# Performance work log

Hardware: AMD Instinct MI355X
Metric: run time of the kernel (lower is better)

## Reference

```python
import jax, jax.numpy as jnp
import numpy as np

N_NODES = 50000
N_EDGES = 800000


def setup_inputs() -> dict:
    key = jax.random.key(0)
    ks = jax.random.split(key, 8)
    x = jax.random.normal(ks[0], (N_NODES, 128), dtype=jnp.float32)
    edge_src = jax.random.randint(ks[1], (N_EDGES,), 0, N_NODES, dtype=jnp.int32)
    edge_dst = jax.random.randint(ks[2], (N_EDGES,), 0, N_NODES, dtype=jnp.int32)
    # normalized-adjacency-style positive edge weights
    edge_weight = jax.random.uniform(ks[3], (N_EDGES,), dtype=jnp.float32)
    # Kipf-style uniform(-stdv, stdv) init, stdv = 1/sqrt(fan_out)
    def w(k, fi, fo):
        stdv = 1.0 / np.sqrt(fo)
        return jax.random.uniform(k, (fi, fo), minval=-stdv, maxval=stdv, dtype=jnp.float32)
    W1 = w(ks[4], 128, 128)
    W2 = w(ks[5], 128, 128)
    W3 = w(ks[6], 128, 64)
    b1 = jnp.zeros((128,), jnp.float32)
    b2 = jnp.zeros((128,), jnp.float32)
    b3 = jnp.zeros((64,), jnp.float32)
    return {"x": x, "edge_src": edge_src, "edge_dst": edge_dst,
            "edge_weight": edge_weight, "W1": W1, "b1": b1,
            "W2": W2, "b2": b2, "W3": W3, "b3": b3}


def reference(x, edge_src, edge_dst, edge_weight, W1, b1, W2, b2, W3, b3):
    N = x.shape[0]

    def graph_conv(h, W, b):
        # support = h @ W  (dense GEMM)
        support = h @ W
        # spmm(adj, support): gather source rows, scale by edge weight,
        # scatter-add into destination rows
        msg = edge_weight[:, None] * support[edge_src]          # [E, d_out]
        agg = jax.ops.segment_sum(msg, edge_dst, num_segments=N)
        return agg + b

    h = jax.nn.relu(graph_conv(x, W1, b1))
    h = jax.nn.relu(graph_conv(h, W2, b2))
    h = graph_conv(h, W3, b3)
    return jax.nn.log_softmax(h, axis=1)
```

## Files before the change

### kernel.cpp

```cpp
#include <hip/hip_runtime.h>
#include <cstdint>
#include <cstddef>

typedef __attribute__((ext_vector_type(8))) short short8v;
typedef __attribute__((ext_vector_type(4))) float f32x4;

__device__ inline uint bf16_rne(float f) {
    uint u = __float_as_uint(f);
    return (u + 0x7fffu + ((u >> 16) & 1u)) >> 16;
}
__device__ inline float bf16lo_to_f(uint v) { return __uint_as_float(v << 16); }
__device__ inline float bf16hi_to_f(uint v) { return __uint_as_float(v & 0xffff0000u); }

#define MAXDEG 64
#define RSV 384
#define EPB 2048

__device__ inline void pack_one(const float* __restrict__ W, ushort* __restrict__ Wp,
                                int NC, int i) {
    int j = i & 7, l = (i >> 3) & 63, kb = (i >> 9) & 3, c = i >> 11;
    int row = kb * 32 + ((l >> 4) & 3) * 8 + j;
    int col = c * 16 + (l & 15);
    Wp[i] = (ushort)bf16_rne(W[row * NC + col]);
}

__global__ __launch_bounds__(256) void part_init_kernel(
        const int* __restrict__ esrc, const int* __restrict__ edst,
        const float* __restrict__ ew, float invN8,
        int* __restrict__ lens, int2* __restrict__ part, int E, int NFB,
        int* __restrict__ cnt, int N,
        const float* __restrict__ W1, ushort* __restrict__ Wp1,
        const float* __restrict__ W2, ushort* __restrict__ Wp2,
        const float* __restrict__ W3, ushort* __restrict__ Wp3) {
    const int b = blockIdx.x;
    if (b >= NFB) {
        const int ZB = (N + 255) >> 8;
        int r = b - NFB;
        if (r < ZB) {
            int i = r * 256 + threadIdx.x;
            if (i < N) cnt[i] = 0;
        } else {
            int p = (r - ZB) * 256 + threadIdx.x;
            if (p < 16384) pack_one(W1, Wp1, 128, p);
            else if (p < 32768) pack_one(W2, Wp2, 128, p - 16384);
            else if (p < 40960) pack_one(W3, Wp3, 64, p - 32768);
        }
        return;
    }
    const int fb = b;
    __shared__ int lcnt[8];
    if (threadIdx.x < 8) lcnt[threadIdx.x] = 0;
    __syncthreads();

    const int lane = threadIdx.x & 63;
    const unsigned long long ltmask = (1ULL << lane) - 1ULL;
    const int base = fb * EPB;

#pragma unroll
    for (int j = 0; j < 8; ++j) {
        int idx = base + j * 256 + threadIdx.x;
        bool valid = idx < E;
        int dv = 0, bk = -1;
        int2 rec;
        if (valid) {
            dv = edst[idx];
            bk = min(7, (int)((float)dv * invN8));
            rec.x = (dv << 16) | esrc[idx];
            rec.y = __float_as_int(ew[idx]);
        }
        int myrank = 0, lanecnt = 0;
#pragma unroll
        for (int k = 0; k < 8; ++k) {
            unsigned long long mk = __ballot(bk == k);
            if (bk == k) myrank = (int)__popcll(mk & ltmask);
            if (lane == k) lanecnt = (int)__popcll(mk);
        }
        int wbase = 0;
        if (lane < 8) wbase = atomicAdd(&lcnt[lane], lanecnt);
        int segbase = __shfl(wbase, (bk < 0) ? 0 : bk);
        if (valid) {
            int pos = segbase + myrank;
            if (pos < RSV) part[((size_t)bk * NFB + fb) * RSV + pos] = rec;
        }
    }
    __syncthreads();
    if (threadIdx.x < 8) lens[fb * 8 + threadIdx.x] = min(lcnt[threadIdx.x], RSV);
}

template <int NC, bool F32IN>
__device__ __forceinline__ void gemm_body(const void* __restrict__ Xin,
                                          const ushort* __restrict__ Wp,
                                          ushort* __restrict__ Out, int M, int bid,
                                          ushort* WL) {
    const int t = threadIdx.x;
    {
        const uint4* srcp = (const uint4*)Wp;
        uint4* dstp = (uint4*)WL;
#pragma unroll
        for (int i = 0; i < NC / 16; ++i) dstp[t + i * 256] = srcp[t + i * 256];
    }
    __syncthreads();

    const int wave = t >> 6, l = t & 63;
    const int lr = l & 15, lh = l >> 4;
    const int rowbase = bid * 64 + wave * 16;
    const int arow_idx = min(rowbase + lr, M - 1);

    short8v a[4];
    if (F32IN) {
        const float* arow = (const float*)Xin + (size_t)arow_idx * 128 + lh * 8;
#pragma unroll
        for (int kb = 0; kb < 4; ++kb) {
            float4 u = *(const float4*)(arow + kb * 32);
            float4 v = *(const float4*)(arow + kb * 32 + 4);
            short8v av;
            av[0] = (short)bf16_rne(u.x); av[1] = (short)bf16_rne(u.y);
            av[2] = (short)bf16_rne(u.z); av[3] = (short)bf16_rne(u.w);
            av[4] = (short)bf16_rne(v.x); av[5] = (short)bf16_rne(v.y);
            av[6] = (short)bf16_rne(v.z); av[7] = (short)bf16_rne(v.w);
            a[kb] = av;
        }
    } else {
        const ushort* arow = (const ushort*)Xin + (size_t)arow_idx * 128 + lh * 8;
#pragma unroll
        for (int kb = 0; kb < 4; ++kb) a[kb] = *(const short8v*)(arow + kb * 32);
    }

    f32x4 acc[NC / 16];
#pragma unroll
    for (int c = 0; c < NC / 16; ++c) acc[c] = (f32x4){0.f, 0.f, 0.f, 0.f};

#pragma unroll
    for (int c = 0; c < NC / 16; ++c)
#pragma unroll
        for (int kb = 0; kb < 4; ++kb) {
            short8v b = *(const short8v*)(WL + ((c * 4 + kb) * 64 + l) * 8);
            acc[c] = __builtin_amdgcn_mfma_f32_16x16x32_bf16(a[kb], b, acc[c], 0, 0, 0);
        }

#pragma unroll
    for (int c = 0; c < NC / 16; ++c)
#pragma unroll
        for (int i = 0; i < 4; ++i) {
            int row = rowbase + lh * 4 + i;
            if (row < M) Out[(size_t)row * NC + c * 16 + lr] = (ushort)bf16_rne(acc[c][i]);
        }
}

template <int NC, bool F32IN>
__global__ __launch_bounds__(256) void gemm_mfma(const void* __restrict__ Xin,
                                                 const ushort* __restrict__ Wp,
                                                 ushort* __restrict__ Out, int M) {
    __shared__ ushort WL[128 * NC];
    gemm_body<NC, F32IN>(Xin, Wp, Out, M, blockIdx.x, WL);
}

__global__ __launch_bounds__(256) void gemm1_scatter_kernel(
        const float* __restrict__ X, const ushort* __restrict__ Wp1,
        ushort* __restrict__ Out, int M, int GG, int NSG,
        const int* __restrict__ lens, const int2* __restrict__ part,
        int* __restrict__ cnt, uint* __restrict__ slots, int NFB) {
    __shared__ ushort WL[128 * 128];
    const int g = blockIdx.x >> 3;
    const int i = blockIdx.x & 7;
    if (((g & 1) == 0) && ((g >> 1) < GG)) {
        gemm_body<128, true>(X, Wp1, Out, M, (g >> 1) * 8 + i, WL);
        return;
    }
    const int gemms_before = min((g + 1) >> 1, GG);
    const int sg = g - gemms_before;
    const int bucket = i;
    for (int seg = sg; seg < NFB; seg += NSG) {
        const int len = lens[seg * 8 + bucket];
        const int2* p = part + ((size_t)bucket * NFB + seg) * RSV;
        for (int r = threadIdx.x; r < len; r += 256) {
            int2 rec = p[r];
            uint dv = (uint)rec.x >> 16;
            uint src = (uint)rec.x & 0xffffu;
            int pos = atomicAdd(&cnt[dv], 1);
            if (pos < MAXDEG)
                slots[(size_t)dv * MAXDEG + pos] =
                    (bf16_rne(__int_as_float(rec.y)) << 16) | src;
        }
    }
}

__global__ void spmm128_kernel(const uint* __restrict__ S, const int* __restrict__ cnt,
                               const uint* __restrict__ slots, const float* __restrict__ bias,
                               uint* __restrict__ Out, int N) {
    const int bucket = blockIdx.x & 7;
    const int bidx = blockIdx.x >> 3;
    const int lo = (int)((long)bucket * N / 8);
    const int hi = (int)((long)(bucket + 1) * N / 8);
    const int node = lo + bidx * 4 + (threadIdx.x >> 6);
    const int lane = threadIdx.x & 63;
    if (node >= hi) return;
    const int e1 = min(cnt[node], MAXDEG);
    const uint* sl = slots + (size_t)node * MAXDEG;
    float ax = 0.f, ay = 0.f;
    int e = 0;

#define EDGE128(pk)                                                  \
    {                                                                \
        uint _p = (pk);                                              \
        float _w = __uint_as_float(_p & 0xffff0000u);                \
        uint _v = S[(size_t)(_p & 0xffffu) * 64 + lane];             \
        ax = fmaf(_w, bf16lo_to_f(_v), ax);                          \
        ay = fmaf(_w, bf16hi_to_f(_v), ay);                          \
    }

    for (; e + 8 <= e1; e += 8) {
        uint4 c0 = *(const uint4*)(sl + e);
        uint4 c1 = *(const uint4*)(sl + e + 4);
        EDGE128(c0.x); EDGE128(c0.y); EDGE128(c0.z); EDGE128(c0.w);
        EDGE128(c1.x); EDGE128(c1.y); EDGE128(c1.z); EDGE128(c1.w);
    }
    for (; e + 4 <= e1; e += 4) {
        uint4 c0 = *(const uint4*)(sl + e);
        EDGE128(c0.x); EDGE128(c0.y); EDGE128(c0.z); EDGE128(c0.w);
    }
    for (; e < e1; ++e) EDGE128(sl[e]);
#undef EDGE128

    float2 bv = ((const float2*)bias)[lane];
    ax = fmaxf(ax + bv.x, 0.f);
    ay = fmaxf(ay + bv.y, 0.f);
    Out[(size_t)node * 64 + lane] = (bf16_rne(ay) << 16) | bf16_rne(ax);
}

__global__ void spmm64_kernel(const uint* __restrict__ S32, const int* __restrict__ cnt,
                              const uint* __restrict__ slots, const float* __restrict__ bias,
                              float* __restrict__ Out, int N) {
    const int bucket = blockIdx.x & 7;
    const int bidx = blockIdx.x >> 3;
    const int lo = (int)((long)bucket * N / 8);
    const int hi = (int)((long)(bucket + 1) * N / 8);
    const int node = lo + bidx * 8 + (threadIdx.x >> 5);
    const int l = threadIdx.x & 31;
    if (node >= hi) return;
    const int e1 = min(cnt[node], MAXDEG);
    const uint* sl = slots + (size_t)node * MAXDEG;
    float a0 = 0.f, a1 = 0.f;
    int e = 0;

#define EDGE64(pk)                                                  \
    {                                                               \
        uint _p = (pk);                                             \
        float _w = __uint_as_float(_p & 0xffff0000u);               \
        uint _v = S32[(size_t)(_p & 0xffffu) * 32 + l];             \
        a0 = fmaf(_w, bf16lo_to_f(_v), a0);                         \
        a1 = fmaf(_w, bf16hi_to_f(_v), a1);                         \
    }

    for (; e + 8 <= e1; e += 8) {
        uint4 c0 = *(const uint4*)(sl + e);
        uint4 c1 = *(const uint4*)(sl + e + 4);
        EDGE64(c0.x); EDGE64(c0.y); EDGE64(c0.z); EDGE64(c0.w);
        EDGE64(c1.x); EDGE64(c1.y); EDGE64(c1.z); EDGE64(c1.w);
    }
    for (; e + 4 <= e1; e += 4) {
        uint4 c0 = *(const uint4*)(sl + e);
        EDGE64(c0.x); EDGE64(c0.y); EDGE64(c0.z); EDGE64(c0.w);
    }
    for (; e < e1; ++e) EDGE64(sl[e]);
#undef EDGE64

    float2 bv = ((const float2*)bias)[l];
    float v0 = a0 + bv.x;
    float v1 = a1 + bv.y;
    float m = fmaxf(v0, v1);
#pragma unroll
    for (int d = 16; d >= 1; d >>= 1) m = fmaxf(m, __shfl_xor(m, d));
    float s = __expf(v0 - m) + __expf(v1 - m);
#pragma unroll
    for (int d = 16; d >= 1; d >>= 1) s += __shfl_xor(s, d);
    float ls = __logf(s);
    float2 o;
    o.x = (v0 - m) - ls;
    o.y = (v1 - m) - ls;
    ((float2*)Out)[(size_t)node * 32 + l] = o;
}


extern "C" void kernel_launch(void* const* d_in, const int* in_sizes, int n_in,
                              void* d_out, int out_size, void* d_ws, size_t ws_size,
                              hipStream_t stream) {
    const float* x  = (const float*)d_in[0];
    const int* esrc = (const int*)d_in[1];
    const int* edst = (const int*)d_in[2];
    const float* ew = (const float*)d_in[3];
    const float* W1 = (const float*)d_in[4];
    const float* b1 = (const float*)d_in[5];
    const float* W2 = (const float*)d_in[6];
    const float* b2 = (const float*)d_in[7];
    const float* W3 = (const float*)d_in[8];
    const float* b3 = (const float*)d_in[9];

    const int N = in_sizes[0] / 128;
    const int E = in_sizes[1];

    char* ws = (char*)d_ws;
    auto alloc = [&](size_t bytes) {
        char* p = ws;
        ws += (bytes + 255) & ~(size_t)255;
        return p;
    };
    const int NFB = (E + EPB - 1) / EPB;
    int* cnt     = (int*)alloc((size_t)N * 4);
    int* lens    = (int*)alloc((size_t)(NFB + 8) * 8 * 4);
    uint* slots  = (uint*)alloc((size_t)N * MAXDEG * 4);
    ushort* Sb   = (ushort*)alloc((size_t)N * 128 * 2);
    ushort* Hb   = (ushort*)alloc((size_t)N * 128 * 2);
    ushort* Wp1  = (ushort*)alloc(128 * 128 * 2);
    ushort* Wp2  = (ushort*)alloc(128 * 128 * 2);
    ushort* Wp3  = (ushort*)alloc(128 * 64 * 2);
    (void)ws_size;
    int2* part = (int2*)Hb;

    const float invN8 = 8.0f / (float)N;
    const int ZB = (N + 255) / 256;
    const int PK = (40960 + 255) / 256;

    part_init_kernel<<<NFB + ZB + PK, 256, 0, stream>>>(
        esrc, edst, ew, invN8, lens, part, E, NFB,
        cnt, N, W1, Wp1, W2, Wp2, W3, Wp3);

    const int GB = (N + 63) / 64;
    const int GG = (GB + 7) / 8;
    const int NSG = 128;
    const int TG = GG + NSG;
    gemm1_scatter_kernel<<<TG * 8, 256, 0, stream>>>(
        x, Wp1, Sb, N, GG, NSG, lens, part, cnt, slots, NFB);

    const int bpb128 = (((N + 7) / 8) + 3) / 4;
    spmm128_kernel<<<bpb128 * 8, 256, 0, stream>>>((const uint*)Sb, cnt, slots, b1, (uint*)Hb, N);

    gemm_mfma<128, false><<<GB, 256, 0, stream>>>(Hb, Wp2, Sb, N);
    spmm128_kernel<<<bpb128 * 8, 256, 0, stream>>>((const uint*)Sb, cnt, slots, b2, (uint*)Hb, N);

    gemm_mfma<64, false><<<GB, 256, 0, stream>>>(Hb, Wp3, Sb, N);
    const int bpb64 = (((N + 7) / 8) + 7) / 8;
    spmm64_kernel<<<bpb64 * 8, 256, 0, stream>>>((const uint*)Sb, cnt, slots, b3, (float*)d_out, N);
}
```

Before: 157.1 us.

## Fuse SpMM aggregation with the following layer's MFMA GEMM per 64-node tile

Replaces the separate spmm128 and gemm_mfma launches with one kernel. Each block aggregates 64 nodes into LDS as bf16 with bias and ReLU, then multiplies that tile by the next layer's packed weights using MFMA and writes the support matrix directly. This drops the round trip of the hidden activation through global memory and two kernel launches. In exchange each block reloads the full weight matrix into LDS, uses more LDS per block, and runs at 512 threads, which may lower occupancy for the latency-bound gather.

Result: slower. 161.2 us (+2.6%).

```diff
diff --git a/kernel.cpp b/kernel.cpp
--- a/kernel.cpp
+++ b/kernel.cpp
@@ -147,14 +147,6 @@
         }
 }
 
-template <int NC, bool F32IN>
-__global__ __launch_bounds__(256) void gemm_mfma(const void* __restrict__ Xin,
-                                                 const ushort* __restrict__ Wp,
-                                                 ushort* __restrict__ Out, int M) {
-    __shared__ ushort WL[128 * NC];
-    gemm_body<NC, F32IN>(Xin, Wp, Out, M, blockIdx.x, WL);
-}
-
 __global__ __launch_bounds__(256) void gemm1_scatter_kernel(
         const float* __restrict__ X, const ushort* __restrict__ Wp1,
         ushort* __restrict__ Out, int M, int GG, int NSG,
@@ -185,47 +177,89 @@
     }
 }
 
-__global__ void spmm128_kernel(const uint* __restrict__ S, const int* __restrict__ cnt,
-                               const uint* __restrict__ slots, const float* __restrict__ bias,
-                               uint* __restrict__ Out, int N) {
+template <int NC>
+__global__ __launch_bounds__(512) void spmm_gemm_kernel(
+        const uint* __restrict__ S, const int* __restrict__ cnt,
+        const uint* __restrict__ slots, const float* __restrict__ bias,
+        const ushort* __restrict__ Wp, ushort* __restrict__ Out, int N) {
+    __shared__ uint HL[64][68];
+    __shared__ ushort WL[128 * NC];
+    const int t = threadIdx.x;
+    {
+        const uint4* srcp = (const uint4*)Wp;
+        uint4* dstp = (uint4*)WL;
+#pragma unroll
+        for (int i = 0; i < NC / 32; ++i) dstp[t + i * 512] = srcp[t + i * 512];
+    }
     const int bucket = blockIdx.x & 7;
-    const int bidx = blockIdx.x >> 3;
+    const int tile = blockIdx.x >> 3;
     const int lo = (int)((long)bucket * N / 8);
     const int hi = (int)((long)(bucket + 1) * N / 8);
-    const int node = lo + bidx * 4 + (threadIdx.x >> 6);
-    const int lane = threadIdx.x & 63;
-    if (node >= hi) return;
-    const int e1 = min(cnt[node], MAXDEG);
-    const uint* sl = slots + (size_t)node * MAXDEG;
-    float ax = 0.f, ay = 0.f;
-    int e = 0;
-
+    const int base = lo + tile * 64;
+    const int wave = t >> 6, lane = t & 63;
+
+    float2 bv = ((const float2*)bias)[lane];
+#pragma unroll
+    for (int r8 = 0; r8 < 8; ++r8) {
+        const int r = wave * 8 + r8;
+        const int node = base + r;
+        float ax = 0.f, ay = 0.f;
+        if (node < hi) {
+            const int e1 = min(cnt[node], MAXDEG);
+            const uint* sl = slots + (size_t)node * MAXDEG;
+            int e = 0;
 #define EDGE128(pk)                                                  \
-    {                                                                \
-        uint _p = (pk);                                              \
-        float _w = __uint_as_float(_p & 0xffff0000u);                \
-        uint _v = S[(size_t)(_p & 0xffffu) * 64 + lane];             \
-        ax = fmaf(_w, bf16lo_to_f(_v), ax);                          \
-        ay = fmaf(_w, bf16hi_to_f(_v), ay);                          \
-    }
-
-    for (; e + 8 <= e1; e += 8) {
-        uint4 c0 = *(const uint4*)(sl + e);
-        uint4 c1 = *(const uint4*)(sl + e + 4);
-        EDGE128(c0.x); EDGE128(c0.y); EDGE128(c0.z); EDGE128(c0.w);
-        EDGE128(c1.x); EDGE128(c1.y); EDGE128(c1.z); EDGE128(c1.w);
-    }
-    for (; e + 4 <= e1; e += 4) {
-        uint4 c0 = *(const uint4*)(sl + e);
-        EDGE128(c0.x); EDGE128(c0.y); EDGE128(c0.z); EDGE128(c0.w);
-    }
-    for (; e < e1; ++e) EDGE128(sl[e]);
+            {                                                        \
+                uint _p = (pk);                                      \
+                float _w = __uint_as_float(_p & 0xffff0000u);        \
+                uint _v = S[(size_t)(_p & 0xffffu) * 64 + lane];     \
+                ax = fmaf(_w, bf16lo_to_f(_v), ax);                  \
+                ay = fmaf(_w, bf16hi_to_f(_v), ay);                  \
+            }
+            for (; e + 8 <= e1; e += 8) {
+                uint4 c0 = *(const uint4*)(sl + e);
+                uint4 c1 = *(const uint4*)(sl + e + 4);
+                EDGE128(c0.x); EDGE128(c0.y); EDGE128(c0.z); EDGE128(c0.w);
+                EDGE128(c1.x); EDGE128(c1.y); EDGE128(c1.z); EDGE128(c1.w);
+            }
+            for (; e + 4 <= e1; e += 4) {
+                uint4 c0 = *(const uint4*)(sl + e);
+                EDGE128(c0.x); EDGE128(c0.y); EDGE128(c0.z); EDGE128(c0.w);
+            }
+            for (; e < e1; ++e) EDGE128(sl[e]);
 #undef EDGE128
-
-    float2 bv = ((const float2*)bias)[lane];
-    ax = fmaxf(ax + bv.x, 0.f);
-    ay = fmaxf(ay + bv.y, 0.f);
-    Out[(size_t)node * 64 + lane] = (bf16_rne(ay) << 16) | bf16_rne(ax);
+            ax = fmaxf(ax + bv.x, 0.f);
+            ay = fmaxf(ay + bv.y, 0.f);
+        }
+        HL[r][lane] = (bf16_rne(ay) << 16) | bf16_rne(ax);
+    }
+    __syncthreads();
+
+    const int lr = lane & 15, lh = lane >> 4;
+    const int rt = wave & 3;
+    const int nct = NC / 16;
+    const int ct0 = (wave >> 2) * (nct / 2);
+
+    short8v a[4];
+#pragma unroll
+    for (int kb = 0; kb < 4; ++kb)
+        a[kb] = *(const short8v*)&HL[rt * 16 + lr][kb * 16 + lh * 4];
+
+#pragma unroll
+    for (int c = 0; c < NC / 32; ++c) {
+        const int ct = ct0 + c;
+        f32x4 acc = (f32x4){0.f, 0.f, 0.f, 0.f};
+#pragma unroll
+        for (int kb = 0; kb < 4; ++kb) {
+            short8v b = *(const short8v*)(WL + ((ct * 4 + kb) * 64 + lane) * 8);
+            acc = __builtin_amdgcn_mfma_f32_16x16x32_bf16(a[kb], b, acc, 0, 0, 0);
+        }
+#pragma unroll
+        for (int i = 0; i < 4; ++i) {
+            int row = base + rt * 16 + lh * 4 + i;
+            if (row < hi) Out[(size_t)row * NC + ct * 16 + lr] = (ushort)bf16_rne(acc[i]);
+        }
+    }
 }
 
 __global__ void spmm64_kernel(const uint* __restrict__ S32, const int* __restrict__ cnt,
@@ -332,13 +366,14 @@
     gemm1_scatter_kernel<<<TG * 8, 256, 0, stream>>>(
         x, Wp1, Sb, N, GG, NSG, lens, part, cnt, slots, NFB);
 
-    const int bpb128 = (((N + 7) / 8) + 3) / 4;
-    spmm128_kernel<<<bpb128 * 8, 256, 0, stream>>>((const uint*)Sb, cnt, slots, b1, (uint*)Hb, N);
-
-    gemm_mfma<128, false><<<GB, 256, 0, stream>>>(Hb, Wp2, Sb, N);
-    spmm128_kernel<<<bpb128 * 8, 256, 0, stream>>>((const uint*)Sb, cnt, slots, b2, (uint*)Hb, N);
-
-    gemm_mfma<64, false><<<GB, 256, 0, stream>>>(Hb, Wp3, Sb, N);
+    const int BPB = ((((N + 7) / 8) + 63) / 64);
+    spmm_gemm_kernel<128><<<BPB * 8, 512, 0, stream>>>(
+        (const uint*)Sb, cnt, slots, b1, Wp2, Hb, N);
+
+    spmm_gemm_kernel<64><<<BPB * 8, 512, 0, stream>>>(
+        (const uint*)Hb, cnt, slots, b2, Wp3, Sb, N);
+
     const int bpb64 = (((N + 7) / 8) + 7) / 8;
-    spmm64_kernel<<<bpb64 * 8, 256, 0, stream>>>((const uint*)Sb, cnt, slots, b3, (float*)d_out, N);
-}
+    spmm64_kernel<<<bpb64 * 8, 256, 0, stream>>>(
+        (const uint*)Sb, cnt, slots, b3, (float*)d_out, N);
+}
```
